# Optimization experiments

Hardware: AMD Instinct MI355X
Metric: run time of the kernel (lower is better)

The kernel has to match this reference:

```python
import jax, jax.numpy as jnp
import numpy as np


def _skew(x):
    # Shift row i right by i: [B,C,H,W] -> [B,C,H,W+H-1]
    B, C, H, W = x.shape
    Wn = W + H - 1
    rows = jnp.arange(H)[:, None]           # [H,1]
    cols = rows + jnp.arange(W)[None, :]    # [H,W]
    out = jnp.zeros((B, C, H, Wn), x.dtype)
    return out.at[:, :, rows, cols].set(x)


def _unskew(y, W):
    # Inverse of _skew: [B,C,H,W+H-1] -> [B,C,H,W]
    H = y.shape[2]
    rows = jnp.arange(H)[:, None]
    cols = rows + jnp.arange(W)[None, :]
    return y[:, :, rows, cols]


def setup_inputs() -> dict:
    key = jax.random.key(0)
    k0, k1, k2 = jax.random.split(key, 3)
    B, C, H, W = 32, 128, 32, 32
    s = 1.0 / np.sqrt(C)
    return {
        "x": jax.random.normal(k0, (B, C, H, W), jnp.float32),
        "W_is": jax.random.normal(k1, (4 * C, C), jnp.float32) * s,   # 1x1 conv input->state
        "b_is": jnp.zeros((4 * C,), jnp.float32),
        "W_ss": jax.random.normal(k2, (4 * C, C, 2), jnp.float32) * s,  # conv1d k=2 state->state
        "b_ss": jnp.zeros((4 * C,), jnp.float32),
    }


def reference(x, W_is, b_is, W_ss, b_ss):
    B, C, H, W = x.shape
    xs = _skew(x)  # [B,C,H,Wn]
    # input-to-state: 1x1 conv -> [B,4C,H,Wn]
    i_s = jnp.einsum('bchw,oc->bohw', xs, W_is) + b_is[None, :, None, None]
    i_s_t = jnp.transpose(i_s, (3, 0, 1, 2))  # [Wn,B,4C,H] for scan over width
    W0, W1 = W_ss[:, :, 0], W_ss[:, :, 1]

    def cell(carry, its):
        h, c = carry  # each [B,C,H]
        # prepend zero along height then conv1d(k=2): tap0 sees h shifted down by 1
        h_up = jnp.pad(h, ((0, 0), (0, 0), (1, 0)))[:, :, :-1]
        s_s = (jnp.einsum('bch,oc->boh', h_up, W0)
               + jnp.einsum('bch,oc->boh', h, W1)
               + b_ss[None, :, None])
        z = its + s_s                       # [B,4C,H]
        ofi = jax.nn.sigmoid(z[:, :3 * C])
        g = jnp.tanh(z[:, 3 * C:])
        o, f, i = ofi[:, :C], ofi[:, C:2 * C], ofi[:, 2 * C:]
        c_new = f * c + i * g
        h_new = o * jnp.tanh(c_new)
        return (h_new, c_new), h_new

    init = (jnp.zeros((B, C, H), x.dtype), jnp.zeros((B, C, H), x.dtype))
    _, hs = jax.lax.scan(cell, init, i_s_t)   # hs: [Wn,B,C,H]
    out = jnp.transpose(hs, (1, 2, 3, 0))     # [B,C,H,Wn]
    return _unskew(out, W)
```

## Files before the change

### kernel.cpp

```cpp
#include <hip/hip_runtime.h>

#define B_ 32
#define C_ 128
#define H_ 32
#define W_ 32
#define WN 63
#define O_ 512
#define HTB (33 * 256)
#define BIAS_ROW 32768

typedef __attribute__((ext_vector_type(8))) short bf16x8;
typedef __attribute__((ext_vector_type(4))) float f32x4;
typedef __attribute__((ext_vector_type(4))) unsigned short us4;
typedef __attribute__((ext_vector_type(2))) unsigned int u32x2;

#define L2E 1.442695041f
#define L2E2 2.885390082f

#if __has_builtin(__builtin_amdgcn_exp2f)
__device__ __forceinline__ float EXP2(float x) { return __builtin_amdgcn_exp2f(x); }
#else
__device__ __forceinline__ float EXP2(float x) {
  float r; asm("v_exp_f32 %0, %1" : "=v"(r) : "v"(x)); return r;
}
#endif

__device__ __forceinline__ unsigned cvt_pk_bf16(float lo, float hi) {
  unsigned r;
  asm("v_cvt_pk_bf16_f32 %0, %1, %2" : "=v"(r) : "v"(lo), "v"(hi));
  return r;
}

__device__ __forceinline__ unsigned short f2bf(float f) {
  union { float f; unsigned u; } v; v.f = f;
  unsigned r = v.u + 0x7FFFu + ((v.u >> 16) & 1u);
  return (unsigned short)(r >> 16);
}
__device__ __forceinline__ float bf2f(unsigned short h) {
  union { unsigned u; float f; } v; v.u = ((unsigned)h) << 16;
  return v.f;
}

__device__ __forceinline__ void lds_barrier() {
  __builtin_amdgcn_sched_barrier(0);
  asm volatile("s_waitcnt lgkmcnt(0)" ::: "memory");
  __builtin_amdgcn_s_barrier();
  __builtin_amdgcn_sched_barrier(0);
}

__device__ __forceinline__ int diag_off(int t) {
  return (t <= 31) ? (t * (t + 1) / 2) : (1024 - (63 - t) * (64 - t) / 2);
}

__global__ __launch_bounds__(512, 2)
void is_kernel(const float* __restrict__ x, const float* __restrict__ W_is,
               const float* __restrict__ b_is, const float* __restrict__ b_ss,
               unsigned short* __restrict__ is_ws) {
  const int bid = blockIdx.x;
  const int b = bid >> 3, jq = bid & 7;
  const int tid = threadIdx.x;
  const int w = tid >> 6, l = tid & 63;
  const int lg = l >> 4, lm = l & 15;

  if (bid == 0) {
    float v = (b_is[tid] + b_ss[tid]) * ((tid >> 7) == 3 ? L2E2 : L2E);
    is_ws[(size_t)BIAS_ROW * O_ + tid] = f2bf(v);
  }

  __shared__ __align__(16) unsigned short xT[128 * 128];
#pragma unroll
  for (int it = 0; it < 32; ++it) {
    int idx = it * 512 + tid;
    int c = idx & 31, jl = (idx >> 5) & 3, ch = idx >> 7;
    float v = x[((b * C_ + ch) * H_ + jq * 4 + jl) * W_ + c];
    int rr = jl * 32 + c;
    int byteCol = ch * 2;
    int addr = rr * 256 + (((byteCol >> 4) ^ (rr & 15)) << 4) + (byteCol & 15);
    *(unsigned short*)((char*)xT + addr) = f2bf(v);
  }
  __syncthreads();

  f32x4 acc[4][8];
#pragma unroll
  for (int g = 0; g < 4; ++g)
#pragma unroll
    for (int nt = 0; nt < 8; ++nt) acc[g][nt] = (f32x4){0.f, 0.f, 0.f, 0.f};

#pragma unroll
  for (int kf = 0; kf < 4; ++kf) {
    bf16x8 bfv[8];
#pragma unroll
    for (int nt = 0; nt < 8; ++nt) {
      int rr = (nt >> 1) * 32 + (nt & 1) * 16 + lm;
      int chunk = kf * 4 + lg;
      int addr = rr * 256 + ((chunk ^ (rr & 15)) << 4);
      bfv[nt] = *(const bf16x8*)((const char*)xT + addr);
    }
#pragma unroll
    for (int g = 0; g < 4; ++g) {
      const int o = g * 128 + 16 * w + lm;
      const float* wp = W_is + o * C_ + kf * 32 + lg * 8;
      f32x4 wa = *(const f32x4*)(wp);
      f32x4 wb = *(const f32x4*)(wp + 4);
      bf16x8 af;
      af[0] = (short)f2bf(wa[0]); af[1] = (short)f2bf(wa[1]);
      af[2] = (short)f2bf(wa[2]); af[3] = (short)f2bf(wa[3]);
      af[4] = (short)f2bf(wb[0]); af[5] = (short)f2bf(wb[1]);
      af[6] = (short)f2bf(wb[2]); af[7] = (short)f2bf(wb[3]);
#pragma unroll
      for (int nt = 0; nt < 8; ++nt)
        acc[g][nt] = __builtin_amdgcn_mfma_f32_16x16x32_bf16(af, bfv[nt], acc[g][nt], 0, 0, 0);
    }
  }

#pragma unroll
  for (int g = 0; g < 4; ++g) {
    const float sc = (g == 3) ? L2E2 : L2E;
    const int ob = g * 128 + 16 * w + lg * 4;
#pragma unroll
    for (int nt = 0; nt < 8; ++nt) {
      int jl = nt >> 1;
      int c = (nt & 1) * 16 + lm;
      int j = jq * 4 + jl;
      int t = j + c;
      int jmin = (t > 31) ? (t - 31) : 0;
      us4 st;
#pragma unroll
      for (int r = 0; r < 4; ++r)
        st[r] = f2bf((acc[g][nt][r] + b_is[ob + r] + b_ss[ob + r]) * sc);
      *(us4*)(is_ws + (size_t)(b * 1024 + diag_off(t) + (j - jmin)) * O_ + ob) = st;
    }
  }
}

__global__ __launch_bounds__(512, 2)
void scan_kernel(const float* __restrict__ Wss,
                 unsigned short* __restrict__ is_ws) {
  const int b = blockIdx.x;
  const int tid = threadIdx.x;
  const int w = tid >> 6, l = tid & 63;
  const int lg = l >> 4, lm = l & 15;
  const int chW = 16 * w;
  float* ows = (float*)is_ws;

  __shared__ __align__(16) unsigned short hT[2 * 33 * 128];
  for (int i = tid; i < 2 * 33 * 128; i += 512) hT[i] = 0;

  bf16x8 A[4][8];
#pragma unroll
  for (int g = 0; g < 4; ++g) {
    const float sc = (g == 3) ? L2E2 : L2E;
    const int o = g * 128 + chW + lm;
#pragma unroll
    for (int kf = 0; kf < 4; ++kf) {
      const int ch = kf * 32 + lg * 8;
      const float* wp = Wss + (o * C_ + ch) * 2;
      f32x4 q0 = *(const f32x4*)(wp + 0);
      f32x4 q1 = *(const f32x4*)(wp + 4);
      f32x4 q2 = *(const f32x4*)(wp + 8);
      f32x4 q3 = *(const f32x4*)(wp + 12);
      bf16x8 a0, a1;
      a0[0] = (short)f2bf(q0[0] * sc); a1[0] = (short)f2bf(q0[1] * sc);
      a0[1] = (short)f2bf(q0[2] * sc); a1[1] = (short)f2bf(q0[3] * sc);
      a0[2] = (short)f2bf(q1[0] * sc); a1[2] = (short)f2bf(q1[1] * sc);
      a0[3] = (short)f2bf(q1[2] * sc); a1[3] = (short)f2bf(q1[3] * sc);
      a0[4] = (short)f2bf(q2[0] * sc); a1[4] = (short)f2bf(q2[1] * sc);
      a0[5] = (short)f2bf(q2[2] * sc); a1[5] = (short)f2bf(q2[3] * sc);
      a0[6] = (short)f2bf(q3[0] * sc); a1[6] = (short)f2bf(q3[1] * sc);
      a0[7] = (short)f2bf(q3[2] * sc); a1[7] = (short)f2bf(q3[3] * sc);
      A[g][kf] = a0;
      A[g][kf + 4] = a1;
    }
  }

  float cst[2][4] = {{0.f, 0.f, 0.f, 0.f}, {0.f, 0.f, 0.f, 0.f}};
  us4 isvA[4][2], isvB[4][2];

  auto load_is = [&](int t, us4 (&iv)[4][2]) {
    const int jmin = (t > 31) ? (t - 31) : 0;
    const int dOff = b * 1024 + diag_off(t) - jmin;
#pragma unroll
    for (int n = 0; n < 2; ++n) {
      const int j = n * 16 + lm;
      const bool valid = ((unsigned)(t - j) < 32u);
      const int row = valid ? (dOff + j) : BIAS_ROW;
      const unsigned short* p = is_ws + (size_t)row * O_ + chW + lg * 4;
#pragma unroll
      for (int g = 0; g < 4; ++g) iv[g][n] = *(const us4*)(p + g * 128);
    }
  };

  auto step_body = [&](int t, int rOff, int wOff, us4 (&isv)[4][2],
                       us4 (&isvN)[4][2], bool pf) {
    const int nLo = (t < 47) ? 0 : 1;
    const int jminT = (t > 31) ? (t - 31) : 0;
    const int rowBase = b * 1024 + diag_off(t) - jminT;

    f32x4 acc[4][2];
#pragma unroll
    for (int n = 0; n < 2; ++n) {
      if (n >= nLo) {
#pragma unroll
        for (int g = 0; g < 4; ++g)
#pragma unroll
          for (int r = 0; r < 4; ++r) acc[g][n][r] = bf2f(isv[g][n][r]);
        const int j = n * 16 + lm;
        const int rU = (j == 0) ? 32 : j - 1;
#pragma unroll
        for (int kf = 0; kf < 8; ++kf) {
          const int rr = (kf < 4) ? rU : j;
          const int chunk = (kf & 3) * 4 + lg;
          const int addr = rOff + rr * 256 + ((chunk ^ (rr & 15)) << 4);
          bf16x8 bfv = *(const bf16x8*)((const char*)hT + addr);
#pragma unroll
          for (int g = 0; g < 4; ++g)
            acc[g][n] = __builtin_amdgcn_mfma_f32_16x16x32_bf16(A[g][kf], bfv, acc[g][n], 0, 0, 0);
        }
      }
    }

    if (pf) load_is(t + 1, isvN);

#pragma unroll
    for (int n = 0; n < 2; ++n) {
      if (n >= nLo) {
        const int j = n * 16 + lm;
        const int c = t - j;
        const bool inband = ((unsigned)c < 32u);
        f32x4 ov;
#pragma unroll
        for (int r = 0; r < 4; ++r) {
          float eo = EXP2(-acc[0][n][r]);
          float ef = EXP2(-acc[1][n][r]);
          float ei = EXP2(-acc[2][n][r]);
          float eg = EXP2(-acc[3][n][r]);
          float Af = 1.f + ef, Bi = 1.f + ei, Gg = 1.f + eg;
          float BG = Bi * Gg;
          float num = cst[n][r] * BG + (1.f - eg) * Af;
          float cn = num * __builtin_amdgcn_rcpf(Af * BG);
          cst[n][r] = cn;
          float ec = EXP2(cn * -L2E2);
          float hn = (1.f - ec) * __builtin_amdgcn_rcpf((1.f + ec) * (1.f + eo));
          ov[r] = hn;
        }
        if (inband)
          *(f32x4*)(ows + (size_t)(rowBase + j) * 256 + chW + lg * 4) = ov;
        u32x2 hb;
        hb[0] = cvt_pk_bf16(ov[0], ov[1]);
        hb[1] = cvt_pk_bf16(ov[2], ov[3]);
        const int byteCol = chW * 2 + lg * 8;
        const int chunk = byteCol >> 4;
        const int addr = wOff + j * 256 + ((chunk ^ (j & 15)) << 4) + (byteCol & 15);
        *(u32x2*)((char*)hT + addr) = hb;
      }
    }

    lds_barrier();
  };

  load_is(0, isvA);
  __syncthreads();

  for (int t = 0; t < WN - 1; t += 2) {
    step_body(t, 0, HTB, isvA, isvB, true);
    step_body(t + 1, HTB, 0, isvB, isvA, t + 2 < WN);
  }
  step_body(WN - 1, 0, HTB, isvA, isvB, false);
}

__global__ __launch_bounds__(256, 4)
void unpack_kernel(const float* __restrict__ ows, float* __restrict__ out) {
  const int bid = blockIdx.x;
  const int b = bid >> 5, j = bid & 31;
  const int tid = threadIdx.x;

  __shared__ float tile[32 * 129];

  {
    const int ch = tid & 127;
    const int half = tid >> 7;
#pragma unroll
    for (int q = 0; q < 16; ++q) {
      int c = q * 2 + half;
      int t = j + c;
      int jmin = (t > 31) ? (t - 31) : 0;
      size_t row = (size_t)(b * 1024 + diag_off(t) + (j - jmin));
      tile[c * 129 + ch] = ows[row * 256 + ch];
    }
  }
  __syncthreads();

  {
    const int c = tid & 31;
    const int ch0 = tid >> 5;
#pragma unroll
    for (int q = 0; q < 16; ++q) {
      int ch = q * 8 + ch0;
      out[((size_t)(b * C_ + ch) * H_ + j) * W_ + c] = tile[c * 129 + ch];
    }
  }
}

extern "C" void kernel_launch(void* const* d_in, const int* in_sizes, int n_in,
                              void* d_out, int out_size, void* d_ws, size_t ws_size,
                              hipStream_t stream) {
  const float* x    = (const float*)d_in[0];
  const float* W_is = (const float*)d_in[1];
  const float* b_is = (const float*)d_in[2];
  const float* W_ss = (const float*)d_in[3];
  const float* b_ss = (const float*)d_in[4];
  float* out = (float*)d_out;
  unsigned short* is_ws = (unsigned short*)d_ws;

  is_kernel<<<dim3(B_ * 8), dim3(512), 0, stream>>>(x, W_is, b_is, b_ss, is_ws);
  scan_kernel<<<dim3(B_), dim3(512), 0, stream>>>(W_ss, is_ws);
  unpack_kernel<<<dim3(B_ * H_), dim3(256), 0, stream>>>((const float*)is_ws, out);
}
```

Measured before the change: 178.9 us.

## Split scan recurrence K across paired waves with LDS partial-sum exchange

The scan kernel doubles its block to 1024 threads, so each pair of waves splits the state-to-state matmul by conv tap. One wave computes the tap-0 product and the other the tap-1 product, each for both row halves. Partial sums for the other wave's rows go through a new dynamic-LDS exchange buffer, and each wave then runs the gate math only for its own 16 rows. This halves the per-wave MFMA chain and transcendental work on the serial critical path of each timestep. In exchange it adds an extra barrier and an LDS round trip per step, and it drops the software prefetch of the next step's input-to-state values.

```diff
diff --git a/kernel.cpp b/kernel.cpp
--- a/kernel.cpp
+++ b/kernel.cpp
@@ -8,6 +8,8 @@
 #define O_ 512
 #define HTB (33 * 256)
 #define BIAS_ROW 32768
+#define PEXCH_OFF (2 * 33 * 256)
+#define SCAN_LDS (PEXCH_OFF + 65536)
 
 typedef __attribute__((ext_vector_type(8))) short bf16x8;
 typedef __attribute__((ext_vector_type(4))) float f32x4;
@@ -133,20 +135,28 @@
   }
 }
 
-__global__ __launch_bounds__(512, 2)
+__global__ __launch_bounds__(1024, 4)
 void scan_kernel(const float* __restrict__ Wss,
                  unsigned short* __restrict__ is_ws) {
+  extern __shared__ __align__(16) char lds[];
+  unsigned short* hT = (unsigned short*)lds;
+  char* pexch = lds + PEXCH_OFF;
+
   const int b = blockIdx.x;
   const int tid = threadIdx.x;
-  const int w = tid >> 6, l = tid & 63;
+  const int v = tid >> 6;
+  const int kh = v & 1;
+  const int w = v >> 1;
+  const int l = tid & 63;
   const int lg = l >> 4, lm = l & 15;
   const int chW = 16 * w;
+  const int jOwn = kh * 16 + lm;
+  const int jOth = (kh ^ 1) * 16 + lm;
   float* ows = (float*)is_ws;
 
-  __shared__ __align__(16) unsigned short hT[2 * 33 * 128];
-  for (int i = tid; i < 2 * 33 * 128; i += 512) hT[i] = 0;
-
-  bf16x8 A[4][8];
+  for (int i = tid; i < 2 * 33 * 128; i += 1024) hT[i] = 0;
+
+  bf16x8 A[4][4];
 #pragma unroll
   for (int g = 0; g < 4; ++g) {
     const float sc = (g == 3) ? L2E2 : L2E;
@@ -154,118 +164,134 @@
 #pragma unroll
     for (int kf = 0; kf < 4; ++kf) {
       const int ch = kf * 32 + lg * 8;
-      const float* wp = Wss + (o * C_ + ch) * 2;
-      f32x4 q0 = *(const f32x4*)(wp + 0);
-      f32x4 q1 = *(const f32x4*)(wp + 4);
-      f32x4 q2 = *(const f32x4*)(wp + 8);
-      f32x4 q3 = *(const f32x4*)(wp + 12);
-      bf16x8 a0, a1;
-      a0[0] = (short)f2bf(q0[0] * sc); a1[0] = (short)f2bf(q0[1] * sc);
-      a0[1] = (short)f2bf(q0[2] * sc); a1[1] = (short)f2bf(q0[3] * sc);
-      a0[2] = (short)f2bf(q1[0] * sc); a1[2] = (short)f2bf(q1[1] * sc);
-      a0[3] = (short)f2bf(q1[2] * sc); a1[3] = (short)f2bf(q1[3] * sc);
-      a0[4] = (short)f2bf(q2[0] * sc); a1[4] = (short)f2bf(q2[1] * sc);
-      a0[5] = (short)f2bf(q2[2] * sc); a1[5] = (short)f2bf(q2[3] * sc);
-      a0[6] = (short)f2bf(q3[0] * sc); a1[6] = (short)f2bf(q3[1] * sc);
-      a0[7] = (short)f2bf(q3[2] * sc); a1[7] = (short)f2bf(q3[3] * sc);
-      A[g][kf] = a0;
-      A[g][kf + 4] = a1;
-    }
-  }
-
-  float cst[2][4] = {{0.f, 0.f, 0.f, 0.f}, {0.f, 0.f, 0.f, 0.f}};
-  us4 isvA[4][2], isvB[4][2];
-
-  auto load_is = [&](int t, us4 (&iv)[4][2]) {
-    const int jmin = (t > 31) ? (t - 31) : 0;
-    const int dOff = b * 1024 + diag_off(t) - jmin;
-#pragma unroll
-    for (int n = 0; n < 2; ++n) {
-      const int j = n * 16 + lm;
-      const bool valid = ((unsigned)(t - j) < 32u);
-      const int row = valid ? (dOff + j) : BIAS_ROW;
-      const unsigned short* p = is_ws + (size_t)row * O_ + chW + lg * 4;
-#pragma unroll
-      for (int g = 0; g < 4; ++g) iv[g][n] = *(const us4*)(p + g * 128);
-    }
-  };
-
-  auto step_body = [&](int t, int rOff, int wOff, us4 (&isv)[4][2],
-                       us4 (&isvN)[4][2], bool pf) {
-    const int nLo = (t < 47) ? 0 : 1;
+      const float* wp = Wss + (o * C_ + ch) * 2 + kh;
+      bf16x8 a;
+      a[0] = (short)f2bf(wp[0]  * sc);
+      a[1] = (short)f2bf(wp[2]  * sc);
+      a[2] = (short)f2bf(wp[4]  * sc);
+      a[3] = (short)f2bf(wp[6]  * sc);
+      a[4] = (short)f2bf(wp[8]  * sc);
+      a[5] = (short)f2bf(wp[10] * sc);
+      a[6] = (short)f2bf(wp[12] * sc);
+      a[7] = (short)f2bf(wp[14] * sc);
+      A[g][kf] = a;
+    }
+  }
+
+  const int rrOwn = kh ? jOwn : ((jOwn == 0) ? 32 : jOwn - 1);
+  const int rrOth = kh ? jOth : (jOth - 1);
+
+  const int exWr = (w * 8 + kh * 4) * 1024 + l * 16;
+  const int exRd = (w * 8 + (kh ^ 1) * 4) * 1024 + l * 16;
+
+  const int exWrB = (w * 8 + ((kh ^ 1) * 4)) * 1024 + l * 16;
+  const int exRdB = (w * 8 + (kh * 4)) * 1024 + l * 16;
+
+  int wAddrLane;
+  {
+    int byteCol = chW * 2 + lg * 8;
+    wAddrLane = jOwn * 256 + (((byteCol >> 4) ^ (jOwn & 15)) << 4) + (byteCol & 15);
+  }
+
+  float cst[4] = {0.f, 0.f, 0.f, 0.f};
+
+  __syncthreads();
+
+  auto step_body = [&](int t, int rOff, int wOff) {
+    const bool ownActive = (t < 47) || (kh == 1);
+    const bool othActive = (t < 47) || (kh == 0);
     const int jminT = (t > 31) ? (t - 31) : 0;
     const int rowBase = b * 1024 + diag_off(t) - jminT;
 
-    f32x4 acc[4][2];
-#pragma unroll
-    for (int n = 0; n < 2; ++n) {
-      if (n >= nLo) {
+    f32x4 accOwn[4], accOth[4];
+#pragma unroll
+    for (int g = 0; g < 4; ++g) {
+      accOwn[g] = (f32x4){0.f, 0.f, 0.f, 0.f};
+      accOth[g] = (f32x4){0.f, 0.f, 0.f, 0.f};
+    }
+
+    if (othActive) {
+#pragma unroll
+      for (int kf = 0; kf < 4; ++kf) {
+        const int chunk = kf * 4 + lg;
+        const int addr = rOff + rrOth * 256 + ((chunk ^ (rrOth & 15)) << 4);
+        bf16x8 bfv = *(const bf16x8*)((const char*)hT + addr);
 #pragma unroll
         for (int g = 0; g < 4; ++g)
-#pragma unroll
-          for (int r = 0; r < 4; ++r) acc[g][n][r] = bf2f(isv[g][n][r]);
-        const int j = n * 16 + lm;
-        const int rU = (j == 0) ? 32 : j - 1;
-#pragma unroll
-        for (int kf = 0; kf < 8; ++kf) {
-          const int rr = (kf < 4) ? rU : j;
-          const int chunk = (kf & 3) * 4 + lg;
-          const int addr = rOff + rr * 256 + ((chunk ^ (rr & 15)) << 4);
-          bf16x8 bfv = *(const bf16x8*)((const char*)hT + addr);
-#pragma unroll
-          for (int g = 0; g < 4; ++g)
-            acc[g][n] = __builtin_amdgcn_mfma_f32_16x16x32_bf16(A[g][kf], bfv, acc[g][n], 0, 0, 0);
-        }
+          accOth[g] = __builtin_amdgcn_mfma_f32_16x16x32_bf16(A[g][kf], bfv, accOth[g], 0, 0, 0);
       }
     }
-
-    if (pf) load_is(t + 1, isvN);
-
-#pragma unroll
-    for (int n = 0; n < 2; ++n) {
-      if (n >= nLo) {
-        const int j = n * 16 + lm;
-        const int c = t - j;
-        const bool inband = ((unsigned)c < 32u);
-        f32x4 ov;
-#pragma unroll
-        for (int r = 0; r < 4; ++r) {
-          float eo = EXP2(-acc[0][n][r]);
-          float ef = EXP2(-acc[1][n][r]);
-          float ei = EXP2(-acc[2][n][r]);
-          float eg = EXP2(-acc[3][n][r]);
-          float Af = 1.f + ef, Bi = 1.f + ei, Gg = 1.f + eg;
-          float BG = Bi * Gg;
-          float num = cst[n][r] * BG + (1.f - eg) * Af;
-          float cn = num * __builtin_amdgcn_rcpf(Af * BG);
-          cst[n][r] = cn;
-          float ec = EXP2(cn * -L2E2);
-          float hn = (1.f - ec) * __builtin_amdgcn_rcpf((1.f + ec) * (1.f + eo));
-          ov[r] = hn;
-        }
-        if (inband)
-          *(f32x4*)(ows + (size_t)(rowBase + j) * 256 + chW + lg * 4) = ov;
-        u32x2 hb;
-        hb[0] = cvt_pk_bf16(ov[0], ov[1]);
-        hb[1] = cvt_pk_bf16(ov[2], ov[3]);
-        const int byteCol = chW * 2 + lg * 8;
-        const int chunk = byteCol >> 4;
-        const int addr = wOff + j * 256 + ((chunk ^ (j & 15)) << 4) + (byteCol & 15);
-        *(u32x2*)((char*)hT + addr) = hb;
+    if (ownActive) {
+#pragma unroll
+      for (int kf = 0; kf < 4; ++kf) {
+        const int chunk = kf * 4 + lg;
+        const int addr = rOff + rrOwn * 256 + ((chunk ^ (rrOwn & 15)) << 4);
+        bf16x8 bfv = *(const bf16x8*)((const char*)hT + addr);
+#pragma unroll
+        for (int g = 0; g < 4; ++g)
+          accOwn[g] = __builtin_amdgcn_mfma_f32_16x16x32_bf16(A[g][kf], bfv, accOwn[g], 0, 0, 0);
       }
+    }
+
+    us4 isv[4];
+    if (ownActive) {
+      const bool valid = ((unsigned)(t - jOwn) < 32u);
+      const int row = valid ? (rowBase + jOwn) : BIAS_ROW;
+      const unsigned short* p = is_ws + (size_t)row * O_ + chW + lg * 4;
+#pragma unroll
+      for (int g = 0; g < 4; ++g) isv[g] = *(const us4*)(p + g * 128);
+    }
+
+    if (othActive) {
+#pragma unroll
+      for (int g = 0; g < 4; ++g)
+        *(f32x4*)(pexch + exWrB + g * 1024) = accOth[g];
+    }
+
+    lds_barrier();
+
+    if (ownActive) {
+      const int c = t - jOwn;
+      const bool inband = ((unsigned)c < 32u);
+      f32x4 ov;
+#pragma unroll
+      for (int g = 0; g < 4; ++g) {
+        f32x4 pg = *(const f32x4*)(pexch + exRdB + g * 1024);
+#pragma unroll
+        for (int r = 0; r < 4; ++r)
+          accOwn[g][r] += pg[r] + bf2f(isv[g][r]);
+      }
+#pragma unroll
+      for (int r = 0; r < 4; ++r) {
+        float eo = EXP2(-accOwn[0][r]);
+        float ef = EXP2(-accOwn[1][r]);
+        float ei = EXP2(-accOwn[2][r]);
+        float eg = EXP2(-accOwn[3][r]);
+        float Af = 1.f + ef, Bi = 1.f + ei, Gg = 1.f + eg;
+        float BG = Bi * Gg;
+        float num = cst[r] * BG + (1.f - eg) * Af;
+        float cn = num * __builtin_amdgcn_rcpf(Af * BG);
+        cst[r] = cn;
+        float ec = EXP2(cn * -L2E2);
+        float hn = (1.f - ec) * __builtin_amdgcn_rcpf((1.f + ec) * (1.f + eo));
+        ov[r] = hn;
+      }
+      if (inband)
+        *(f32x4*)(ows + (size_t)(rowBase + jOwn) * 256 + chW + lg * 4) = ov;
+      u32x2 hb;
+      hb[0] = cvt_pk_bf16(ov[0], ov[1]);
+      hb[1] = cvt_pk_bf16(ov[2], ov[3]);
+      *(u32x2*)((char*)hT + wOff + wAddrLane) = hb;
     }
 
     lds_barrier();
   };
 
-  load_is(0, isvA);
-  __syncthreads();
-
   for (int t = 0; t < WN - 1; t += 2) {
-    step_body(t, 0, HTB, isvA, isvB, true);
-    step_body(t + 1, HTB, 0, isvB, isvA, t + 2 < WN);
-  }
-  step_body(WN - 1, 0, HTB, isvA, isvB, false);
+    step_body(t, 0, HTB);
+    step_body(t + 1, HTB, 0);
+  }
+  step_body(WN - 1, 0, HTB);
 }
 
 __global__ __launch_bounds__(256, 4)
@@ -312,7 +338,9 @@
   float* out = (float*)d_out;
   unsigned short* is_ws = (unsigned short*)d_ws;
 
+  (void)hipFuncSetAttribute((const void*)scan_kernel,
+                            hipFuncAttributeMaxDynamicSharedMemorySize, SCAN_LDS);
   is_kernel<<<dim3(B_ * 8), dim3(512), 0, stream>>>(x, W_is, b_is, b_ss, is_ws);
-  scan_kernel<<<dim3(B_), dim3(512), 0, stream>>>(W_ss, is_ws);
+  scan_kernel<<<dim3(B_), dim3(1024), SCAN_LDS, stream>>>(W_ss, is_ws);
   unpack_kernel<<<dim3(B_ * H_), dim3(256), 0, stream>>>((const float*)is_ws, out);
 }
```

Result: slower. 260.0 us (+45.3%).

## Process two batches per scan block to interleave independent recurrences

Applied to the files above, without the earlier changes.

The scan kernel now runs two batch elements per workgroup, launching half as many blocks, so the two independent recurrences can interleave their MFMA and transcendental work and hide each other's latency. The input-state loads are no longer prefetched one step ahead; they are issued at the start of each step and added after the matmul. This halves the number of CUs used, on a GPU that already had only 32 blocks, and lengthens the serial work per block. The exposed global load latency per step is also a risk.

```diff
diff --git a/kernel.cpp b/kernel.cpp
--- a/kernel.cpp
+++ b/kernel.cpp
@@ -7,6 +7,7 @@
 #define WN 63
 #define O_ 512
 #define HTB (33 * 256)
+#define HTB2 (2 * HTB)
 #define BIAS_ROW 32768
 
 typedef __attribute__((ext_vector_type(8))) short bf16x8;
@@ -136,15 +137,15 @@
 __global__ __launch_bounds__(512, 2)
 void scan_kernel(const float* __restrict__ Wss,
                  unsigned short* __restrict__ is_ws) {
-  const int b = blockIdx.x;
+  const int b0 = blockIdx.x * 2;
   const int tid = threadIdx.x;
   const int w = tid >> 6, l = tid & 63;
   const int lg = l >> 4, lm = l & 15;
   const int chW = 16 * w;
   float* ows = (float*)is_ws;
 
-  __shared__ __align__(16) unsigned short hT[2 * 33 * 128];
-  for (int i = tid; i < 2 * 33 * 128; i += 512) hT[i] = 0;
+  __shared__ __align__(16) unsigned short hT[2 * 2 * 33 * 128];
+  for (int i = tid; i < 2 * 2 * 33 * 128; i += 512) hT[i] = 0;
 
   bf16x8 A[4][8];
 #pragma unroll
@@ -173,44 +174,26 @@
     }
   }
 
-  float cst[2][4] = {{0.f, 0.f, 0.f, 0.f}, {0.f, 0.f, 0.f, 0.f}};
-  us4 isvA[4][2], isvB[4][2];
-
-  auto load_is = [&](int t, us4 (&iv)[4][2]) {
-    const int jmin = (t > 31) ? (t - 31) : 0;
-    const int dOff = b * 1024 + diag_off(t) - jmin;
-#pragma unroll
-    for (int n = 0; n < 2; ++n) {
-      const int j = n * 16 + lm;
-      const bool valid = ((unsigned)(t - j) < 32u);
-      const int row = valid ? (dOff + j) : BIAS_ROW;
-      const unsigned short* p = is_ws + (size_t)row * O_ + chW + lg * 4;
-#pragma unroll
-      for (int g = 0; g < 4; ++g) iv[g][n] = *(const us4*)(p + g * 128);
-    }
-  };
-
-  auto step_body = [&](int t, int rOff, int wOff, us4 (&isv)[4][2],
-                       us4 (&isvN)[4][2], bool pf) {
-    const int nLo = (t < 47) ? 0 : 1;
-    const int jminT = (t > 31) ? (t - 31) : 0;
-    const int rowBase = b * 1024 + diag_off(t) - jminT;
-
+  float cst0[2][4] = {{0.f, 0.f, 0.f, 0.f}, {0.f, 0.f, 0.f, 0.f}};
+  float cst1[2][4] = {{0.f, 0.f, 0.f, 0.f}, {0.f, 0.f, 0.f, 0.f}};
+
+  __syncthreads();
+
+  auto half_step = [&](int t, int nLo, int rowBase, int batOff, int rOff,
+                       int wOff, us4 (&isv)[4][2], float (&cst)[2][4]) {
     f32x4 acc[4][2];
 #pragma unroll
     for (int n = 0; n < 2; ++n) {
       if (n >= nLo) {
 #pragma unroll
-        for (int g = 0; g < 4; ++g)
-#pragma unroll
-          for (int r = 0; r < 4; ++r) acc[g][n][r] = bf2f(isv[g][n][r]);
+        for (int g = 0; g < 4; ++g) acc[g][n] = (f32x4){0.f, 0.f, 0.f, 0.f};
         const int j = n * 16 + lm;
         const int rU = (j == 0) ? 32 : j - 1;
 #pragma unroll
         for (int kf = 0; kf < 8; ++kf) {
           const int rr = (kf < 4) ? rU : j;
           const int chunk = (kf & 3) * 4 + lg;
-          const int addr = rOff + rr * 256 + ((chunk ^ (rr & 15)) << 4);
+          const int addr = batOff + rOff + rr * 256 + ((chunk ^ (rr & 15)) << 4);
           bf16x8 bfv = *(const bf16x8*)((const char*)hT + addr);
 #pragma unroll
           for (int g = 0; g < 4; ++g)
@@ -218,8 +201,6 @@
         }
       }
     }
-
-    if (pf) load_is(t + 1, isvN);
 
 #pragma unroll
     for (int n = 0; n < 2; ++n) {
@@ -230,10 +211,14 @@
         f32x4 ov;
 #pragma unroll
         for (int r = 0; r < 4; ++r) {
-          float eo = EXP2(-acc[0][n][r]);
-          float ef = EXP2(-acc[1][n][r]);
-          float ei = EXP2(-acc[2][n][r]);
-          float eg = EXP2(-acc[3][n][r]);
+          float zo = acc[0][n][r] + bf2f(isv[0][n][r]);
+          float zf = acc[1][n][r] + bf2f(isv[1][n][r]);
+          float zi = acc[2][n][r] + bf2f(isv[2][n][r]);
+          float zg = acc[3][n][r] + bf2f(isv[3][n][r]);
+          float eo = EXP2(-zo);
+          float ef = EXP2(-zf);
+          float ei = EXP2(-zi);
+          float eg = EXP2(-zg);
           float Af = 1.f + ef, Bi = 1.f + ei, Gg = 1.f + eg;
           float BG = Bi * Gg;
           float num = cst[n][r] * BG + (1.f - eg) * Af;
@@ -243,29 +228,54 @@
           float hn = (1.f - ec) * __builtin_amdgcn_rcpf((1.f + ec) * (1.f + eo));
           ov[r] = hn;
         }
-        if (inband)
-          *(f32x4*)(ows + (size_t)(rowBase + j) * 256 + chW + lg * 4) = ov;
         u32x2 hb;
         hb[0] = cvt_pk_bf16(ov[0], ov[1]);
         hb[1] = cvt_pk_bf16(ov[2], ov[3]);
         const int byteCol = chW * 2 + lg * 8;
         const int chunk = byteCol >> 4;
-        const int addr = wOff + j * 256 + ((chunk ^ (j & 15)) << 4) + (byteCol & 15);
+        const int addr = batOff + wOff + j * 256 + ((chunk ^ (j & 15)) << 4) + (byteCol & 15);
         *(u32x2*)((char*)hT + addr) = hb;
+        if (inband)
+          *(f32x4*)(ows + (size_t)(rowBase + j) * 256 + chW + lg * 4) = ov;
       }
     }
+  };
+
+  auto load_is = [&](int rowBase, us4 (&iv)[4][2], int t, int nLo) {
+#pragma unroll
+    for (int n = 0; n < 2; ++n) {
+      if (n >= nLo) {
+        const int j = n * 16 + lm;
+        const bool valid = ((unsigned)(t - j) < 32u);
+        const int row = valid ? (rowBase + j) : BIAS_ROW;
+        const unsigned short* p = is_ws + (size_t)row * O_ + chW + lg * 4;
+#pragma unroll
+        for (int g = 0; g < 4; ++g) iv[g][n] = *(const us4*)(p + g * 128);
+      }
+    }
+  };
+
+  auto step_body = [&](int t, int rOff, int wOff) {
+    const int nLo = (t < 47) ? 0 : 1;
+    const int jminT = (t > 31) ? (t - 31) : 0;
+    const int rowBase0 = b0 * 1024 + diag_off(t) - jminT;
+    const int rowBase1 = rowBase0 + 1024;
+
+    us4 isv0[4][2], isv1[4][2];
+    load_is(rowBase0, isv0, t, nLo);
+    load_is(rowBase1, isv1, t, nLo);
+
+    half_step(t, nLo, rowBase0, 0,    rOff, wOff, isv0, cst0);
+    half_step(t, nLo, rowBase1, HTB2, rOff, wOff, isv1, cst1);
 
     lds_barrier();
   };
 
-  load_is(0, isvA);
-  __syncthreads();
-
   for (int t = 0; t < WN - 1; t += 2) {
-    step_body(t, 0, HTB, isvA, isvB, true);
-    step_body(t + 1, HTB, 0, isvB, isvA, t + 2 < WN);
-  }
-  step_body(WN - 1, 0, HTB, isvA, isvB, false);
+    step_body(t, 0, HTB);
+    step_body(t + 1, HTB, 0);
+  }
+  step_body(WN - 1, 0, HTB);
 }
 
 __global__ __launch_bounds__(256, 4)
@@ -313,6 +323,6 @@
   unsigned short* is_ws = (unsigned short*)d_ws;
 
   is_kernel<<<dim3(B_ * 8), dim3(512), 0, stream>>>(x, W_is, b_is, b_ss, is_ws);
-  scan_kernel<<<dim3(B_), dim3(512), 0, stream>>>(W_ss, is_ws);
+  scan_kernel<<<dim3(B_ / 2), dim3(512), 0, stream>>>(W_ss, is_ws);
   unpack_kernel<<<dim3(B_ * H_), dim3(256), 0, stream>>>((const float*)is_ws, out);
 }
```

Result: slower. 335.8 us (+87.6%).
